# Optimization experiments

Measured on AMD Instinct MI355X. Metric: run time of the kernel, lower is better.

## Reference

```python
import jax, jax.numpy as jnp
import numpy as np
import math

NUM_EXPERTS = 8
MIN_EXPERTS_ACTIVE = 2  # max(1, 8 // 4) per __init__ formula


def setup_inputs() -> dict:
    key = jax.random.key(0)
    ks = jax.random.split(key, 6)
    N, Cin, H, W = 16384, 68, 8, 8
    Cproj = 128
    patch = jax.random.normal(ks[0], (N, Cin, H, W), dtype=jnp.float32)
    conv_w = jax.random.normal(ks[1], (Cproj, Cin, 3, 3), dtype=jnp.float32) * (1.0 / np.sqrt(Cin * 9))
    conv_b = jnp.zeros((Cproj,), dtype=jnp.float32)
    fc_w = jax.random.normal(ks[2], (Cproj, NUM_EXPERTS), dtype=jnp.float32) * (1.0 / np.sqrt(Cproj))
    fc_b = jnp.zeros((NUM_EXPERTS,), dtype=jnp.float32)
    wth_max_c = jnp.float32(0.4)
    wth_entropy_c = jnp.float32(0.3)
    wth_gap_c = jnp.float32(0.3)
    threshold = jnp.float32(0.2)
    return {
        'patch': patch, 'conv_w': conv_w, 'conv_b': conv_b,
        'fc_w': fc_w, 'fc_b': fc_b,
        'wth_max_c': wth_max_c, 'wth_entropy_c': wth_entropy_c, 'wth_gap_c': wth_gap_c,
        'threshold': threshold, 'layer_idx': 0, 'current_epoch': 30,
    }


def _gate(patch, conv_w, conv_b, fc_w, fc_b):
    # 3x3 SAME conv (NCHW) -> ReLU -> global avg pool -> linear
    y = jax.lax.conv_general_dilated(
        patch, conv_w, window_strides=(1, 1), padding='SAME',
        dimension_numbers=('NCHW', 'OIHW', 'NCHW'))
    y = jax.nn.relu(y + conv_b[None, :, None, None])
    pooled = y.mean(axis=(2, 3))  # [N, Cproj]
    return pooled @ fc_w + fc_b   # [N, E]


def _compute_gap(sw):
    # sw: [N, E] sorted descending
    k = min(4, NUM_EXPERTS - 1)
    mean_rest = sw[:, 1:k + 1].mean(axis=-1, keepdims=True)
    gap = (sw[:, 0:1] - mean_rest) / (sw[:, 0:1] + 1e-8)
    return jnp.clip(gap, 0.0, 1.0)


def _adaptive_threshold(w, base_threshold, wth_max_c, wth_entropy_c, wth_gap_c):
    sw = -jnp.sort(-w, axis=-1)  # descending
    max_component = 1.0 - sw[:, 0:1]
    mean_w = w.mean(axis=-1, keepdims=True)
    std_w = w.std(axis=-1, keepdims=True, ddof=1)  # torch default unbiased
    entropy = -(w * jnp.log(w + 1e-18)).sum(axis=-1, keepdims=True)
    entropy_component = 1.0 - entropy / math.log(NUM_EXPERTS)
    gap_component = _compute_gap(sw)
    adaptive_factor = (wth_max_c * max_component + wth_entropy_c * entropy_component
                       + wth_gap_c * gap_component)
    th = base_threshold * (0.5 + adaptive_factor)
    min_th = jnp.maximum(jnp.float32(0.05), mean_w - 0.5 * std_w)
    max_th = jnp.minimum(jnp.float32(0.7), sw[:, 0:1] - 0.1 * std_w)
    th = jnp.clip(th, min_th, max_th)
    kth = sw[:, MIN_EXPERTS_ACTIVE - 1:MIN_EXPERTS_ACTIVE]
    return jnp.minimum(th, kth * 0.9)


def reference(patch, conv_w, conv_b, fc_w, fc_b,
              wth_max_c, wth_entropy_c, wth_gap_c,
              threshold, layer_idx, current_epoch):
    logits = _gate(patch, conv_w, conv_b, fc_w, fc_b)
    weights = jax.nn.softmax(logits, axis=-1)
    th = _adaptive_threshold(weights, threshold, wth_max_c, wth_entropy_c, wth_gap_c)
    if current_epoch is not None and current_epoch < 20:
        weights_norm = jnp.ones_like(weights) / NUM_EXPERTS
    elif current_epoch is not None and 20 <= current_epoch <= 25:
        tau = max(0.1, 1.0 - (current_epoch - 20) * 0.18)
        s = jax.nn.sigmoid((weights - th) / tau)
        weights_norm = s / jnp.clip(s.sum(axis=-1, keepdims=True), 1e-8)
    else:  # current_epoch > 25 or eval: straight-through hard/soft masking
        tau = 0.1
        hard = (weights > th).astype(weights.dtype)
        soft = jax.nn.sigmoid((weights - th) / tau)
        filtered = hard + jax.lax.stop_gradient(soft - hard)
        weights_norm = filtered / jnp.clip(filtered.sum(axis=-1, keepdims=True), 1e-8)
    return weights_norm
```

## Files before the change

kernel.cpp:

```cpp
#include <hip/hip_runtime.h>


typedef _Float16 half8 __attribute__((ext_vector_type(8)));
typedef float    floatx4 __attribute__((ext_vector_type(4)));

#define A_SAMPLE  14400
#define LDS_P_OFF 57600
#define LDS_TOTAL 59648

__global__ void prep_weights(const float* __restrict__ cw, _Float16* __restrict__ Bw) {
  int i = blockIdx.x * 256 + threadIdx.x;
  int co = i / 672;
  int k  = i - co * 672;
  int s  = k / 72;
  int ci = k - s * 72;
  float v = 0.f;
  if (s < 9 && ci < 68) {
    int ky = s / 3, kx = s - 3 * ky;
    v = cw[((co * 68 + ci) * 3 + ky) * 3 + kx];
  }
  Bw[i] = (_Float16)v;
}

__global__ __launch_bounds__(256, 2) void router_main(
    const float* __restrict__ patch,
    const float* __restrict__ conv_b,
    const _Float16* __restrict__ Bw,
    const float* __restrict__ fc_w,
    const float* __restrict__ fc_b,
    const float* __restrict__ p_wmax,
    const float* __restrict__ p_went,
    const float* __restrict__ p_wgap,
    const float* __restrict__ p_thr,
    const int* __restrict__ p_epoch,
    float* __restrict__ out)
{
  __shared__ __align__(16) unsigned char lds[LDS_TOTAL];
  const int tid    = threadIdx.x;
  const int l      = tid & 63;
  const int w      = tid >> 6;
  const int lane15 = l & 15;
  const int quad   = l >> 4;
  const int m_half = w >> 1;
  const int n0     = (w & 1) * 64;
  const int n_s    = blockIdx.x * 4;

  {
    unsigned char* abase = lds + w * A_SAMPLE;
    float4 z4 = make_float4(0.f, 0.f, 0.f, 0.f);
    #pragma unroll
    for (int j = 0; j < 15; ++j) {
      int idx = j * 64 + l;
      if (idx < 900) *(float4*)(abase + idx * 16) = z4;
    }
  }
  {
    const float* psrc = patch + (size_t)(n_s + w) * 4352 + l;
    int y = l >> 3, x = l & 7;
    unsigned char* arow = lds + w * A_SAMPLE + ((y + 1) * 10 + (x + 1)) * 144;
    #pragma unroll
    for (int b = 0; b < 9; ++b) {
      half8 h;
      #pragma unroll
      for (int j = 0; j < 8; ++j) {
        int ci = b * 8 + j;
        float v = (ci < 68) ? psrc[ci * 64] : 0.f;
        h[j] = (_Float16)v;
      }
      *(half8*)(arow + b * 16) = h;
    }
  }
  __syncthreads();

  int apos[8];
  #pragma unroll
  for (int t = 0; t < 8; ++t) {
    int p  = (t & 3) * 16 + lane15;
    int pp = ((p >> 3) + 1) * 10 + (p & 7) + 1;
    apos[t] = (m_half * 2 + (t >> 2)) * A_SAMPLE + pp * 144;
  }

  const _Float16* bptr[4];
  #pragma unroll
  for (int n = 0; n < 4; ++n)
    bptr[n] = Bw + (size_t)(n0 + n * 16 + lane15) * 672 + quad * 8;

  floatx4 acc[8][4];
  floatx4 zacc = {0.f, 0.f, 0.f, 0.f};
  #pragma unroll
  for (int t = 0; t < 8; ++t)
    #pragma unroll
    for (int n = 0; n < 4; ++n) acc[t][n] = zacc;

  half8 bcur[4];
  #pragma unroll
  for (int n = 0; n < 4; ++n) bcur[n] = *(const half8*)(bptr[n]);

  #pragma unroll 4
  for (int c = 0; c < 20; ++c) {
    half8 bnext[4];
    #pragma unroll
    for (int n = 0; n < 4; ++n)
      bnext[n] = *(const half8*)(bptr[n] + (c + 1) * 32);

    int kb  = c * 4 + quad;
    int s   = (kb * 57) >> 9;
    int rem = kb - s * 9;
    int dy  = (s * 11) >> 5;
    int dx  = s - 3 * dy;
    int roff = (dy * 10 + dx - 11) * 144 + rem * 16;

    half8 afr[8];
    #pragma unroll
    for (int t = 0; t < 8; ++t)
      afr[t] = *(const half8*)(lds + apos[t] + roff);

    #pragma unroll
    for (int t = 0; t < 8; ++t)
      #pragma unroll
      for (int n = 0; n < 4; ++n)
        acc[t][n] = __builtin_amdgcn_mfma_f32_16x16x32_f16(afr[t], bcur[n], acc[t][n], 0, 0, 0);

    #pragma unroll
    for (int n = 0; n < 4; ++n) bcur[n] = bnext[n];
  }

  {
    int roff = (quad == 0) ? 1712 : 0;
    half8 afr[8];
    #pragma unroll
    for (int t = 0; t < 8; ++t)
      afr[t] = *(const half8*)(lds + apos[t] + roff);
    #pragma unroll
    for (int t = 0; t < 8; ++t)
      #pragma unroll
      for (int n = 0; n < 4; ++n)
        acc[t][n] = __builtin_amdgcn_mfma_f32_16x16x32_f16(afr[t], bcur[n], acc[t][n], 0, 0, 0);
  }

  float bcoef[4];
  #pragma unroll
  for (int n = 0; n < 4; ++n) bcoef[n] = conv_b[n0 + n * 16 + lane15];

  float* pl = (float*)(lds + LDS_P_OFF);
  #pragma unroll
  for (int gl = 0; gl < 2; ++gl) {
    #pragma unroll
    for (int n = 0; n < 4; ++n) {
      float ssum = 0.f;
      #pragma unroll
      for (int tt = 0; tt < 4; ++tt) {
        int t = gl * 4 + tt;
        #pragma unroll
        for (int r = 0; r < 4; ++r)
          ssum += fmaxf(acc[t][n][r] + bcoef[n], 0.f);
      }
      ssum += __shfl_xor(ssum, 16);
      ssum += __shfl_xor(ssum, 32);
      if (l < 16) {
        int g = m_half * 2 + gl;
        pl[g * 128 + n0 + n * 16 + lane15] = ssum * (1.f / 64.f);
      }
    }
  }
  __syncthreads();

  const float* plw = pl + w * 128;
  int e  = l >> 3;
  int c8 = l & 7;
  float part = 0.f;
  #pragma unroll
  for (int m = 0; m < 16; ++m) {
    int co = c8 + 8 * m;
    part += plw[co] * fc_w[co * 8 + e];
  }
  part += __shfl_xor(part, 1);
  part += __shfl_xor(part, 2);
  part += __shfl_xor(part, 4);

  float lg[8];
  #pragma unroll
  for (int j = 0; j < 8; ++j) lg[j] = __shfl(part, j * 8) + fc_b[j];

  float mx = lg[0];
  #pragma unroll
  for (int j = 1; j < 8; ++j) mx = fmaxf(mx, lg[j]);
  float wgt[8]; float sum = 0.f;
  #pragma unroll
  for (int j = 0; j < 8; ++j) { wgt[j] = expf(lg[j] - mx); sum += wgt[j]; }
  float inv = 1.f / sum;
  #pragma unroll
  for (int j = 0; j < 8; ++j) wgt[j] *= inv;

  float sw[8];
  #pragma unroll
  for (int j = 0; j < 8; ++j) sw[j] = wgt[j];
  #define CSD(i, j) { float hi_ = fmaxf(sw[i], sw[j]); float lo_ = fminf(sw[i], sw[j]); sw[i] = hi_; sw[j] = lo_; }
  CSD(0,1) CSD(2,3) CSD(4,5) CSD(6,7)
  CSD(0,2) CSD(1,3) CSD(4,6) CSD(5,7)
  CSD(1,2) CSD(5,6)
  CSD(0,4) CSD(1,5) CSD(2,6) CSD(3,7)
  CSD(2,4) CSD(3,5)
  CSD(1,2) CSD(3,4) CSD(5,6)
  #undef CSD

  float s1 = 0.f;
  #pragma unroll
  for (int j = 0; j < 8; ++j) s1 += wgt[j];
  float mean = s1 * 0.125f;
  float var = 0.f;
  #pragma unroll
  for (int j = 0; j < 8; ++j) { float d = wgt[j] - mean; var += d * d; }
  float stdv = sqrtf(var * (1.f / 7.f));
  float ent = 0.f;
  #pragma unroll
  for (int j = 0; j < 8; ++j) ent -= wgt[j] * logf(wgt[j] + 1e-18f);

  float maxc  = 1.f - sw[0];
  float entc  = 1.f - ent * 0.48089834696298783f;
  float mrest = (sw[1] + sw[2] + sw[3] + sw[4]) * 0.25f;
  float gap   = (sw[0] - mrest) / (sw[0] + 1e-8f);
  gap = fminf(fmaxf(gap, 0.f), 1.f);
  float af = p_wmax[0] * maxc + p_went[0] * entc + p_wgap[0] * gap;
  float th = p_thr[0] * (0.5f + af);
  float mn  = fmaxf(0.05f, mean - 0.5f * stdv);
  float mxt = fminf(0.7f, sw[0] - 0.1f * stdv);
  th = fminf(fmaxf(th, mn), mxt);
  th = fminf(th, sw[1] * 0.9f);

  int epoch = p_epoch[0];
  float outv[8];
  if (epoch < 20) {
    #pragma unroll
    for (int j = 0; j < 8; ++j) outv[j] = 0.125f;
  } else {
    float tau = (epoch <= 25) ? fmaxf(0.1f, 1.0f - (float)(epoch - 20) * 0.18f) : 0.1f;
    float ssum = 0.f;
    #pragma unroll
    for (int j = 0; j < 8; ++j) {
      float sj = 1.f / (1.f + expf(-(wgt[j] - th) / tau));
      outv[j] = sj; ssum += sj;
    }
    float invs = 1.f / fmaxf(ssum, 1e-8f);
    #pragma unroll
    for (int j = 0; j < 8; ++j) outv[j] *= invs;
  }

  if (l < 8) {
    float mv = outv[0];
    #pragma unroll
    for (int j = 1; j < 8; ++j) mv = (l == j) ? outv[j] : mv;
    out[(n_s + w) * 8 + l] = mv;
  }
}

extern "C" void kernel_launch(void* const* d_in, const int* in_sizes, int n_in,
                              void* d_out, int out_size, void* d_ws, size_t ws_size,
                              hipStream_t stream) {
  const float* patch  = (const float*)d_in[0];
  const float* conv_w = (const float*)d_in[1];
  const float* conv_b = (const float*)d_in[2];
  const float* fc_w   = (const float*)d_in[3];
  const float* fc_b   = (const float*)d_in[4];
  const float* wmax   = (const float*)d_in[5];
  const float* went   = (const float*)d_in[6];
  const float* wgap   = (const float*)d_in[7];
  const float* thr    = (const float*)d_in[8];
  const int*   epoch  = (const int*)d_in[10];
  float* outp = (float*)d_out;
  _Float16* Bw = (_Float16*)d_ws;

  int N = in_sizes[0] / 4352;
  prep_weights<<<336, 256, 0, stream>>>(conv_w, Bw);
  router_main<<<N / 4, 256, 0, stream>>>(patch, conv_b, Bw, fc_w, fc_b,
                                         wmax, went, wgap, thr, epoch, outp);
}
```

Before: 496.2 us.

## Halve samples per block to raise occupancy and double-buffer weight fragments

Each block now processes 2 samples instead of 4, with each wave owning one sample and half the output channels. This halves the LDS footprint and accumulator registers so launch bounds can ask for 4 blocks per CU. The K loop is also unrolled in pairs with explicit ping-pong B registers. In exchange, each conv weight fragment fetched from global/L2 is reused across half as many samples, half the waves sit idle during input staging and the tail softmax, and an extra barrier is added after zeroing.

```diff
diff --git a/kernel.cpp b/kernel.cpp
--- a/kernel.cpp
+++ b/kernel.cpp
@@ -5,8 +5,8 @@
 typedef float    floatx4 __attribute__((ext_vector_type(4)));
 
 #define A_SAMPLE  14400
-#define LDS_P_OFF 57600
-#define LDS_TOTAL 59648
+#define LDS_P_OFF 28800
+#define LDS_TOTAL 29824
 
 __global__ void prep_weights(const float* __restrict__ cw, _Float16* __restrict__ Bw) {
   int i = blockIdx.x * 256 + threadIdx.x;
@@ -22,7 +22,7 @@
   Bw[i] = (_Float16)v;
 }
 
-__global__ __launch_bounds__(256, 2) void router_main(
+__global__ __launch_bounds__(256, 4) void router_main(
     const float* __restrict__ patch,
     const float* __restrict__ conv_b,
     const _Float16* __restrict__ Bw,
@@ -41,20 +41,20 @@
   const int w      = tid >> 6;
   const int lane15 = l & 15;
   const int quad   = l >> 4;
-  const int m_half = w >> 1;
+  const int smp    = w >> 1;
   const int n0     = (w & 1) * 64;
-  const int n_s    = blockIdx.x * 4;
+  const int n_s    = blockIdx.x * 2;
 
   {
-    unsigned char* abase = lds + w * A_SAMPLE;
     float4 z4 = make_float4(0.f, 0.f, 0.f, 0.f);
     #pragma unroll
-    for (int j = 0; j < 15; ++j) {
-      int idx = j * 64 + l;
-      if (idx < 900) *(float4*)(abase + idx * 16) = z4;
-    }
-  }
-  {
+    for (int j = 0; j < 8; ++j) {
+      int idx = j * 256 + tid;
+      if (idx < 1800) *(float4*)(lds + idx * 16) = z4;
+    }
+  }
+  __syncthreads();
+  if (w < 2) {
     const float* psrc = patch + (size_t)(n_s + w) * 4352 + l;
     int y = l >> 3, x = l & 7;
     unsigned char* arow = lds + w * A_SAMPLE + ((y + 1) * 10 + (x + 1)) * 144;
@@ -72,12 +72,12 @@
   }
   __syncthreads();
 
-  int apos[8];
-  #pragma unroll
-  for (int t = 0; t < 8; ++t) {
-    int p  = (t & 3) * 16 + lane15;
+  int apos[4];
+  #pragma unroll
+  for (int t = 0; t < 4; ++t) {
+    int p  = t * 16 + lane15;
     int pp = ((p >> 3) + 1) * 10 + (p & 7) + 1;
-    apos[t] = (m_half * 2 + (t >> 2)) * A_SAMPLE + pp * 144;
+    apos[t] = smp * A_SAMPLE + pp * 144;
   }
 
   const _Float16* bptr[4];
@@ -85,57 +85,76 @@
   for (int n = 0; n < 4; ++n)
     bptr[n] = Bw + (size_t)(n0 + n * 16 + lane15) * 672 + quad * 8;
 
-  floatx4 acc[8][4];
+  floatx4 acc[4][4];
   floatx4 zacc = {0.f, 0.f, 0.f, 0.f};
   #pragma unroll
-  for (int t = 0; t < 8; ++t)
+  for (int t = 0; t < 4; ++t)
     #pragma unroll
     for (int n = 0; n < 4; ++n) acc[t][n] = zacc;
 
-  half8 bcur[4];
-  #pragma unroll
-  for (int n = 0; n < 4; ++n) bcur[n] = *(const half8*)(bptr[n]);
-
-  #pragma unroll 4
-  for (int c = 0; c < 20; ++c) {
-    half8 bnext[4];
+  half8 b0[4], b1[4];
+  #pragma unroll
+  for (int n = 0; n < 4; ++n) b0[n] = *(const half8*)(bptr[n]);
+
+  #pragma unroll
+  for (int cc = 0; cc < 10; ++cc) {
+    const int c0 = 2 * cc, c1 = 2 * cc + 1, c2 = 2 * cc + 2;
     #pragma unroll
     for (int n = 0; n < 4; ++n)
-      bnext[n] = *(const half8*)(bptr[n] + (c + 1) * 32);
-
-    int kb  = c * 4 + quad;
-    int s   = (kb * 57) >> 9;
-    int rem = kb - s * 9;
-    int dy  = (s * 11) >> 5;
-    int dx  = s - 3 * dy;
-    int roff = (dy * 10 + dx - 11) * 144 + rem * 16;
-
-    half8 afr[8];
-    #pragma unroll
-    for (int t = 0; t < 8; ++t)
-      afr[t] = *(const half8*)(lds + apos[t] + roff);
-
-    #pragma unroll
-    for (int t = 0; t < 8; ++t)
-      #pragma unroll
-      for (int n = 0; n < 4; ++n)
-        acc[t][n] = __builtin_amdgcn_mfma_f32_16x16x32_f16(afr[t], bcur[n], acc[t][n], 0, 0, 0);
-
-    #pragma unroll
-    for (int n = 0; n < 4; ++n) bcur[n] = bnext[n];
+      b1[n] = *(const half8*)(bptr[n] + c1 * 32);
+
+    {
+      int kb  = c0 * 4 + quad;
+      int s   = (kb * 57) >> 9;
+      int rem = kb - s * 9;
+      int dy  = (s * 11) >> 5;
+      int dx  = s - 3 * dy;
+      int roff = (dy * 10 + dx - 11) * 144 + rem * 16;
+      half8 afr[4];
+      #pragma unroll
+      for (int t = 0; t < 4; ++t)
+        afr[t] = *(const half8*)(lds + apos[t] + roff);
+      #pragma unroll
+      for (int t = 0; t < 4; ++t)
+        #pragma unroll
+        for (int n = 0; n < 4; ++n)
+          acc[t][n] = __builtin_amdgcn_mfma_f32_16x16x32_f16(afr[t], b0[n], acc[t][n], 0, 0, 0);
+    }
+
+    #pragma unroll
+    for (int n = 0; n < 4; ++n)
+      b0[n] = *(const half8*)(bptr[n] + c2 * 32);
+
+    {
+      int kb  = c1 * 4 + quad;
+      int s   = (kb * 57) >> 9;
+      int rem = kb - s * 9;
+      int dy  = (s * 11) >> 5;
+      int dx  = s - 3 * dy;
+      int roff = (dy * 10 + dx - 11) * 144 + rem * 16;
+      half8 afr[4];
+      #pragma unroll
+      for (int t = 0; t < 4; ++t)
+        afr[t] = *(const half8*)(lds + apos[t] + roff);
+      #pragma unroll
+      for (int t = 0; t < 4; ++t)
+        #pragma unroll
+        for (int n = 0; n < 4; ++n)
+          acc[t][n] = __builtin_amdgcn_mfma_f32_16x16x32_f16(afr[t], b1[n], acc[t][n], 0, 0, 0);
+    }
   }
 
   {
     int roff = (quad == 0) ? 1712 : 0;
-    half8 afr[8];
-    #pragma unroll
-    for (int t = 0; t < 8; ++t)
+    half8 afr[4];
+    #pragma unroll
+    for (int t = 0; t < 4; ++t)
       afr[t] = *(const half8*)(lds + apos[t] + roff);
     #pragma unroll
-    for (int t = 0; t < 8; ++t)
+    for (int t = 0; t < 4; ++t)
       #pragma unroll
       for (int n = 0; n < 4; ++n)
-        acc[t][n] = __builtin_amdgcn_mfma_f32_16x16x32_f16(afr[t], bcur[n], acc[t][n], 0, 0, 0);
+        acc[t][n] = __builtin_amdgcn_mfma_f32_16x16x32_f16(afr[t], b0[n], acc[t][n], 0, 0, 0);
   }
 
   float bcoef[4];
@@ -144,113 +163,108 @@
 
   float* pl = (float*)(lds + LDS_P_OFF);
   #pragma unroll
-  for (int gl = 0; gl < 2; ++gl) {
-    #pragma unroll
-    for (int n = 0; n < 4; ++n) {
+  for (int n = 0; n < 4; ++n) {
+    float ssum = 0.f;
+    #pragma unroll
+    for (int t = 0; t < 4; ++t)
+      #pragma unroll
+      for (int r = 0; r < 4; ++r)
+        ssum += fmaxf(acc[t][n][r] + bcoef[n], 0.f);
+    ssum += __shfl_xor(ssum, 16);
+    ssum += __shfl_xor(ssum, 32);
+    if (l < 16)
+      pl[smp * 128 + n0 + n * 16 + lane15] = ssum * (1.f / 64.f);
+  }
+  __syncthreads();
+
+  if (w < 2) {
+    const float* plw = pl + w * 128;
+    int e  = l >> 3;
+    int c8 = l & 7;
+    float part = 0.f;
+    #pragma unroll
+    for (int m = 0; m < 16; ++m) {
+      int co = c8 + 8 * m;
+      part += plw[co] * fc_w[co * 8 + e];
+    }
+    part += __shfl_xor(part, 1);
+    part += __shfl_xor(part, 2);
+    part += __shfl_xor(part, 4);
+
+    float lg[8];
+    #pragma unroll
+    for (int j = 0; j < 8; ++j) lg[j] = __shfl(part, j * 8) + fc_b[j];
+
+    float mx = lg[0];
+    #pragma unroll
+    for (int j = 1; j < 8; ++j) mx = fmaxf(mx, lg[j]);
+    float wgt[8]; float sum = 0.f;
+    #pragma unroll
+    for (int j = 0; j < 8; ++j) { wgt[j] = expf(lg[j] - mx); sum += wgt[j]; }
+    float inv = 1.f / sum;
+    #pragma unroll
+    for (int j = 0; j < 8; ++j) wgt[j] *= inv;
+
+    float sw[8];
+    #pragma unroll
+    for (int j = 0; j < 8; ++j) sw[j] = wgt[j];
+    #define CSD(i, j) { float hi_ = fmaxf(sw[i], sw[j]); float lo_ = fminf(sw[i], sw[j]); sw[i] = hi_; sw[j] = lo_; }
+    CSD(0,1) CSD(2,3) CSD(4,5) CSD(6,7)
+    CSD(0,2) CSD(1,3) CSD(4,6) CSD(5,7)
+    CSD(1,2) CSD(5,6)
+    CSD(0,4) CSD(1,5) CSD(2,6) CSD(3,7)
+    CSD(2,4) CSD(3,5)
+    CSD(1,2) CSD(3,4) CSD(5,6)
+    #undef CSD
+
+    float s1 = 0.f;
+    #pragma unroll
+    for (int j = 0; j < 8; ++j) s1 += wgt[j];
+    float mean = s1 * 0.125f;
+    float var = 0.f;
+    #pragma unroll
+    for (int j = 0; j < 8; ++j) { float d = wgt[j] - mean; var += d * d; }
+    float stdv = sqrtf(var * (1.f / 7.f));
+    float ent = 0.f;
+    #pragma unroll
+    for (int j = 0; j < 8; ++j) ent -= wgt[j] * logf(wgt[j] + 1e-18f);
+
+    float maxc  = 1.f - sw[0];
+    float entc  = 1.f - ent * 0.48089834696298783f;
+    float mrest = (sw[1] + sw[2] + sw[3] + sw[4]) * 0.25f;
+    float gap   = (sw[0] - mrest) / (sw[0] + 1e-8f);
+    gap = fminf(fmaxf(gap, 0.f), 1.f);
+    float af = p_wmax[0] * maxc + p_went[0] * entc + p_wgap[0] * gap;
+    float th = p_thr[0] * (0.5f + af);
+    float mn  = fmaxf(0.05f, mean - 0.5f * stdv);
+    float mxt = fminf(0.7f, sw[0] - 0.1f * stdv);
+    th = fminf(fmaxf(th, mn), mxt);
+    th = fminf(th, sw[1] * 0.9f);
+
+    int epoch = p_epoch[0];
+    float outv[8];
+    if (epoch < 20) {
+      #pragma unroll
+      for (int j = 0; j < 8; ++j) outv[j] = 0.125f;
+    } else {
+      float tau = (epoch <= 25) ? fmaxf(0.1f, 1.0f - (float)(epoch - 20) * 0.18f) : 0.1f;
       float ssum = 0.f;
       #pragma unroll
-      for (int tt = 0; tt < 4; ++tt) {
-        int t = gl * 4 + tt;
-        #pragma unroll
-        for (int r = 0; r < 4; ++r)
-          ssum += fmaxf(acc[t][n][r] + bcoef[n], 0.f);
+      for (int j = 0; j < 8; ++j) {
+        float sj = 1.f / (1.f + expf(-(wgt[j] - th) / tau));
+        outv[j] = sj; ssum += sj;
       }
-      ssum += __shfl_xor(ssum, 16);
-      ssum += __shfl_xor(ssum, 32);
-      if (l < 16) {
-        int g = m_half * 2 + gl;
-        pl[g * 128 + n0 + n * 16 + lane15] = ssum * (1.f / 64.f);
-      }
-    }
-  }
-  __syncthreads();
-
-  const float* plw = pl + w * 128;
-  int e  = l >> 3;
-  int c8 = l & 7;
-  float part = 0.f;
-  #pragma unroll
-  for (int m = 0; m < 16; ++m) {
-    int co = c8 + 8 * m;
-    part += plw[co] * fc_w[co * 8 + e];
-  }
-  part += __shfl_xor(part, 1);
-  part += __shfl_xor(part, 2);
-  part += __shfl_xor(part, 4);
-
-  float lg[8];
-  #pragma unroll
-  for (int j = 0; j < 8; ++j) lg[j] = __shfl(part, j * 8) + fc_b[j];
-
-  float mx = lg[0];
-  #pragma unroll
-  for (int j = 1; j < 8; ++j) mx = fmaxf(mx, lg[j]);
-  float wgt[8]; float sum = 0.f;
-  #pragma unroll
-  for (int j = 0; j < 8; ++j) { wgt[j] = expf(lg[j] - mx); sum += wgt[j]; }
-  float inv = 1.f / sum;
-  #pragma unroll
-  for (int j = 0; j < 8; ++j) wgt[j] *= inv;
-
-  float sw[8];
-  #pragma unroll
-  for (int j = 0; j < 8; ++j) sw[j] = wgt[j];
-  #define CSD(i, j) { float hi_ = fmaxf(sw[i], sw[j]); float lo_ = fminf(sw[i], sw[j]); sw[i] = hi_; sw[j] = lo_; }
-  CSD(0,1) CSD(2,3) CSD(4,5) CSD(6,7)
-  CSD(0,2) CSD(1,3) CSD(4,6) CSD(5,7)
-  CSD(1,2) CSD(5,6)
-  CSD(0,4) CSD(1,5) CSD(2,6) CSD(3,7)
-  CSD(2,4) CSD(3,5)
-  CSD(1,2) CSD(3,4) CSD(5,6)
-  #undef CSD
-
-  float s1 = 0.f;
-  #pragma unroll
-  for (int j = 0; j < 8; ++j) s1 += wgt[j];
-  float mean = s1 * 0.125f;
-  float var = 0.f;
-  #pragma unroll
-  for (int j = 0; j < 8; ++j) { float d = wgt[j] - mean; var += d * d; }
-  float stdv = sqrtf(var * (1.f / 7.f));
-  float ent = 0.f;
-  #pragma unroll
-  for (int j = 0; j < 8; ++j) ent -= wgt[j] * logf(wgt[j] + 1e-18f);
-
-  float maxc  = 1.f - sw[0];
-  float entc  = 1.f - ent * 0.48089834696298783f;
-  float mrest = (sw[1] + sw[2] + sw[3] + sw[4]) * 0.25f;
-  float gap   = (sw[0] - mrest) / (sw[0] + 1e-8f);
-  gap = fminf(fmaxf(gap, 0.f), 1.f);
-  float af = p_wmax[0] * maxc + p_went[0] * entc + p_wgap[0] * gap;
-  float th = p_thr[0] * (0.5f + af);
-  float mn  = fmaxf(0.05f, mean - 0.5f * stdv);
-  float mxt = fminf(0.7f, sw[0] - 0.1f * stdv);
-  th = fminf(fmaxf(th, mn), mxt);
-  th = fminf(th, sw[1] * 0.9f);
-
-  int epoch = p_epoch[0];
-  float outv[8];
-  if (epoch < 20) {
-    #pragma unroll
-    for (int j = 0; j < 8; ++j) outv[j] = 0.125f;
-  } else {
-    float tau = (epoch <= 25) ? fmaxf(0.1f, 1.0f - (float)(epoch - 20) * 0.18f) : 0.1f;
-    float ssum = 0.f;
-    #pragma unroll
-    for (int j = 0; j < 8; ++j) {
-      float sj = 1.f / (1.f + expf(-(wgt[j] - th) / tau));
-      outv[j] = sj; ssum += sj;
-    }
-    float invs = 1.f / fmaxf(ssum, 1e-8f);
-    #pragma unroll
-    for (int j = 0; j < 8; ++j) outv[j] *= invs;
-  }
-
-  if (l < 8) {
-    float mv = outv[0];
-    #pragma unroll
-    for (int j = 1; j < 8; ++j) mv = (l == j) ? outv[j] : mv;
-    out[(n_s + w) * 8 + l] = mv;
+      float invs = 1.f / fmaxf(ssum, 1e-8f);
+      #pragma unroll
+      for (int j = 0; j < 8; ++j) outv[j] *= invs;
+    }
+
+    if (l < 8) {
+      float mv = outv[0];
+      #pragma unroll
+      for (int j = 1; j < 8; ++j) mv = (l == j) ? outv[j] : mv;
+      out[(n_s + w) * 8 + l] = mv;
+    }
   }
 }
 
@@ -272,6 +286,6 @@
 
   int N = in_sizes[0] / 4352;
   prep_weights<<<336, 256, 0, stream>>>(conv_w, Bw);
-  router_main<<<N / 4, 256, 0, stream>>>(patch, conv_b, Bw, fc_w, fc_b,
+  router_main<<<N / 2, 256, 0, stream>>>(patch, conv_b, Bw, fc_w, fc_b,
                                          wmax, went, wgap, thr, epoch, outp);
 }
```

After: 577.9 us. 1.16x slower.

## Switch conv implicit GEMM to 32x32x16 MFMA tiles with double-buffered weights

Applied to the files above, without the earlier changes.

The conv GEMM moves from 16x16x32 MFMA tiles (8x4 tiles per wave) to 32x32x16 MFMA tiles (4x2 per wave). Each chunk now covers the K dimension in two half-steps. Weight fragments are double-buffered with explicit bA/bB ping-pong across a fully unrolled loop. The larger tiles cut the number of LDS A-fragment loads and MFMA issues per FLOP and need only one cross-lane shuffle in the pooling reduction. The trade-off is a different register footprint from the floatx16 accumulators and a full unroll that may raise VGPR pressure under launch_bounds(256,2).

```diff
diff --git a/kernel.cpp b/kernel.cpp
--- a/kernel.cpp
+++ b/kernel.cpp
@@ -2,7 +2,7 @@
 
 
 typedef _Float16 half8 __attribute__((ext_vector_type(8)));
-typedef float    floatx4 __attribute__((ext_vector_type(4)));
+typedef float    floatx16 __attribute__((ext_vector_type(16)));
 
 #define A_SAMPLE  14400
 #define LDS_P_OFF 57600
@@ -20,6 +20,14 @@
     v = cw[((co * 68 + ci) * 3 + ky) * 3 + kx];
   }
   Bw[i] = (_Float16)v;
+}
+
+__device__ __forceinline__ int shift_roff(int kb) {
+  int s   = (kb * 57) >> 9;
+  int rem = kb - s * 9;
+  int dy  = (s * 11) >> 5;
+  int dx  = s - 3 * dy;
+  return (dy * 10 + dx - 11) * 144 + rem * 16;
 }
 
 __global__ __launch_bounds__(256, 2) void router_main(
@@ -39,19 +47,19 @@
   const int tid    = threadIdx.x;
   const int l      = tid & 63;
   const int w      = tid >> 6;
-  const int lane15 = l & 15;
-  const int quad   = l >> 4;
+  const int lane31 = l & 31;
+  const int bhalf  = l >> 5;
   const int m_half = w >> 1;
   const int n0     = (w & 1) * 64;
   const int n_s    = blockIdx.x * 4;
 
   {
-    unsigned char* abase = lds + w * A_SAMPLE;
+    unsigned char* abase0 = lds + w * A_SAMPLE;
     float4 z4 = make_float4(0.f, 0.f, 0.f, 0.f);
     #pragma unroll
     for (int j = 0; j < 15; ++j) {
       int idx = j * 64 + l;
-      if (idx < 900) *(float4*)(abase + idx * 16) = z4;
+      if (idx < 900) *(float4*)(abase0 + idx * 16) = z4;
     }
   }
   {
@@ -72,95 +80,110 @@
   }
   __syncthreads();
 
-  int apos[8];
-  #pragma unroll
-  for (int t = 0; t < 8; ++t) {
-    int p  = (t & 3) * 16 + lane15;
-    int pp = ((p >> 3) + 1) * 10 + (p & 7) + 1;
-    apos[t] = (m_half * 2 + (t >> 2)) * A_SAMPLE + pp * 144;
-  }
-
-  const _Float16* bptr[4];
-  #pragma unroll
-  for (int n = 0; n < 4; ++n)
-    bptr[n] = Bw + (size_t)(n0 + n * 16 + lane15) * 672 + quad * 8;
-
-  floatx4 acc[8][4];
-  floatx4 zacc = {0.f, 0.f, 0.f, 0.f};
-  #pragma unroll
-  for (int t = 0; t < 8; ++t)
-    #pragma unroll
-    for (int n = 0; n < 4; ++n) acc[t][n] = zacc;
-
-  half8 bcur[4];
-  #pragma unroll
-  for (int n = 0; n < 4; ++n) bcur[n] = *(const half8*)(bptr[n]);
-
-  #pragma unroll 4
-  for (int c = 0; c < 20; ++c) {
-    half8 bnext[4];
-    #pragma unroll
-    for (int n = 0; n < 4; ++n)
-      bnext[n] = *(const half8*)(bptr[n] + (c + 1) * 32);
-
-    int kb  = c * 4 + quad;
-    int s   = (kb * 57) >> 9;
-    int rem = kb - s * 9;
-    int dy  = (s * 11) >> 5;
-    int dx  = s - 3 * dy;
-    int roff = (dy * 10 + dx - 11) * 144 + rem * 16;
-
-    half8 afr[8];
-    #pragma unroll
-    for (int t = 0; t < 8; ++t)
-      afr[t] = *(const half8*)(lds + apos[t] + roff);
-
-    #pragma unroll
-    for (int t = 0; t < 8; ++t)
-      #pragma unroll
-      for (int n = 0; n < 4; ++n)
-        acc[t][n] = __builtin_amdgcn_mfma_f32_16x16x32_f16(afr[t], bcur[n], acc[t][n], 0, 0, 0);
-
-    #pragma unroll
-    for (int n = 0; n < 4; ++n) bcur[n] = bnext[n];
-  }
-
+  const unsigned char* abase;
   {
-    int roff = (quad == 0) ? 1712 : 0;
-    half8 afr[8];
-    #pragma unroll
-    for (int t = 0; t < 8; ++t)
-      afr[t] = *(const half8*)(lds + apos[t] + roff);
-    #pragma unroll
-    for (int t = 0; t < 8; ++t)
-      #pragma unroll
-      for (int n = 0; n < 4; ++n)
-        acc[t][n] = __builtin_amdgcn_mfma_f32_16x16x32_f16(afr[t], bcur[n], acc[t][n], 0, 0, 0);
-  }
-
-  float bcoef[4];
-  #pragma unroll
-  for (int n = 0; n < 4; ++n) bcoef[n] = conv_b[n0 + n * 16 + lane15];
+    int pp0 = ((lane31 >> 3) + 1) * 10 + (lane31 & 7) + 1;
+    abase = lds + (m_half * 2) * A_SAMPLE + pp0 * 144;
+  }
+
+  const _Float16* bp[2];
+  #pragma unroll
+  for (int nt = 0; nt < 2; ++nt)
+    bp[nt] = Bw + (size_t)(n0 + nt * 32 + lane31) * 672 + bhalf * 8;
+
+  floatx16 acc[4][2];
+  #pragma unroll
+  for (int mt = 0; mt < 4; ++mt)
+    #pragma unroll
+    for (int nt = 0; nt < 2; ++nt)
+      #pragma unroll
+      for (int r = 0; r < 16; ++r) acc[mt][nt][r] = 0.f;
+
+  half8 bA[4], bB[4];
+  #pragma unroll
+  for (int mi = 0; mi < 2; ++mi)
+    #pragma unroll
+    for (int nt = 0; nt < 2; ++nt)
+      bA[mi * 2 + nt] = *(const half8*)(bp[nt] + mi * 16);
+
+  #define COMPUTE_CHUNK(c, B)                                                     \
+  {                                                                               \
+    int roff0 = shift_roff((c) * 4 + bhalf);                            \
+    int roff1 = shift_roff((c) * 4 + 2 + bhalf);                        \
+    const unsigned char* ap0 = abase + roff0;                                     \
+    const unsigned char* ap1 = abase + roff1;                                     \
+    half8 a0[4], a1[4];                                                           \
+    _Pragma("unroll")                                                             \
+    for (int mt = 0; mt < 4; ++mt)                                                \
+      a0[mt] = *(const half8*)(ap0 + (mt & 1) * 5760 + (mt >> 1) * 14400);        \
+    _Pragma("unroll")                                                             \
+    for (int mt = 0; mt < 4; ++mt)                                                \
+      a1[mt] = *(const half8*)(ap1 + (mt & 1) * 5760 + (mt >> 1) * 14400);        \
+    _Pragma("unroll")                                                             \
+    for (int mt = 0; mt < 4; ++mt)                                                \
+      _Pragma("unroll")                                                           \
+      for (int nt = 0; nt < 2; ++nt)                                              \
+        acc[mt][nt] = __builtin_amdgcn_mfma_f32_32x32x16_f16(a0[mt], B[nt],       \
+                                                             acc[mt][nt], 0, 0, 0); \
+    _Pragma("unroll")                                                             \
+    for (int mt = 0; mt < 4; ++mt)                                                \
+      _Pragma("unroll")                                                           \
+      for (int nt = 0; nt < 2; ++nt)                                              \
+        acc[mt][nt] = __builtin_amdgcn_mfma_f32_32x32x16_f16(a1[mt], B[2 + nt],   \
+                                                             acc[mt][nt], 0, 0, 0); \
+  }
+
+  #pragma unroll
+  for (int cc = 0; cc < 10; ++cc) {
+    const int c0 = 2 * cc, c1 = 2 * cc + 1, c2 = 2 * cc + 2;
+    #pragma unroll
+    for (int mi = 0; mi < 2; ++mi)
+      #pragma unroll
+      for (int nt = 0; nt < 2; ++nt)
+        bB[mi * 2 + nt] = *(const half8*)(bp[nt] + c1 * 32 + mi * 16);
+    COMPUTE_CHUNK(c0, bA)
+    #pragma unroll
+    for (int mi = 0; mi < 2; ++mi)
+      #pragma unroll
+      for (int nt = 0; nt < 2; ++nt)
+        bA[mi * 2 + nt] = *(const half8*)(bp[nt] + c2 * 32 + mi * 16);
+    COMPUTE_CHUNK(c1, bB)
+  }
+  #undef COMPUTE_CHUNK
+
+  {
+    const unsigned char* ap = abase + ((bhalf == 0) ? 1712 : 0);
+    half8 at[4];
+    #pragma unroll
+    for (int mt = 0; mt < 4; ++mt)
+      at[mt] = *(const half8*)(ap + (mt & 1) * 5760 + (mt >> 1) * 14400);
+    #pragma unroll
+    for (int mt = 0; mt < 4; ++mt)
+      #pragma unroll
+      for (int nt = 0; nt < 2; ++nt)
+        acc[mt][nt] = __builtin_amdgcn_mfma_f32_32x32x16_f16(at[mt], bA[nt],
+                                                             acc[mt][nt], 0, 0, 0);
+  }
+
+  float bco[2];
+  #pragma unroll
+  for (int nt = 0; nt < 2; ++nt) bco[nt] = conv_b[n0 + nt * 32 + lane31];
 
   float* pl = (float*)(lds + LDS_P_OFF);
   #pragma unroll
-  for (int gl = 0; gl < 2; ++gl) {
-    #pragma unroll
-    for (int n = 0; n < 4; ++n) {
+  for (int g = 0; g < 2; ++g) {
+    #pragma unroll
+    for (int nt = 0; nt < 2; ++nt) {
       float ssum = 0.f;
       #pragma unroll
-      for (int tt = 0; tt < 4; ++tt) {
-        int t = gl * 4 + tt;
+      for (int mh = 0; mh < 2; ++mh) {
         #pragma unroll
-        for (int r = 0; r < 4; ++r)
-          ssum += fmaxf(acc[t][n][r] + bcoef[n], 0.f);
+        for (int r = 0; r < 16; ++r)
+          ssum += fmaxf(acc[g * 2 + mh][nt][r] + bco[nt], 0.f);
       }
-      ssum += __shfl_xor(ssum, 16);
       ssum += __shfl_xor(ssum, 32);
-      if (l < 16) {
-        int g = m_half * 2 + gl;
-        pl[g * 128 + n0 + n * 16 + lane15] = ssum * (1.f / 64.f);
-      }
+      if (l < 32)
+        pl[(m_half * 2 + g) * 128 + n0 + nt * 32 + lane31] = ssum * (1.f / 64.f);
     }
   }
   __syncthreads();
```

Measured after the change: 507.8 us. +2.3%, slower.
